# Optimization experiments

Hardware: AMD Instinct MI355X
Metric: run time of the kernel (lower is better)

## Reference

```python
import jax, jax.numpy as jnp
from jax import lax
import numpy as np

V, E, H, L = 32000, 512, 1024, 2
B, S, T = 32, 128, 128
PAD = 0


def _lstm_step(h, c, gates):
    i, f, g, o = jnp.split(gates, 4, axis=-1)
    c_new = jax.nn.sigmoid(f) * c + jax.nn.sigmoid(i) * jnp.tanh(g)
    h_new = jax.nn.sigmoid(o) * jnp.tanh(c_new)
    return h_new, c_new


def _lstm_layer(x_tbe, Wih, Whh, bih, bhh):
    # x_tbe: [T, B, in]; returns hs [T, B, H], final (h, c)
    Bn = x_tbe.shape[1]
    Hn = Whh.shape[1]
    h0 = jnp.zeros((Bn, Hn), x_tbe.dtype)
    c0 = jnp.zeros((Bn, Hn), x_tbe.dtype)

    def step(carry, x_t):
        h, c = carry
        gates = x_t @ Wih.T + h @ Whh.T + (bih + bhh)
        h, c = _lstm_step(h, c, gates)
        return (h, c), h

    (h, c), hs = lax.scan(step, (h0, c0), x_tbe)
    return hs, h, c


def setup_inputs() -> dict:
    key = jax.random.key(0)
    ks = iter(jax.random.split(key, 32))
    s = 0.02

    def p(shape):
        return (jax.random.normal(next(ks), shape, dtype=jnp.float32) * s)

    embed = p((V, E)).at[PAD].set(0.0)  # padding_idx row zeroed
    inp = {
        'src': jax.random.randint(next(ks), (B, S), 0, V),
        'tgt': jax.random.randint(next(ks), (B, T), 0, V),
        'embed': embed,
        'enc_Wih0': p((4 * H, E)), 'enc_Whh0': p((4 * H, H)),
        'enc_bih0': p((4 * H,)), 'enc_bhh0': p((4 * H,)),
        'enc_Wih1': p((4 * H, H)), 'enc_Whh1': p((4 * H, H)),
        'enc_bih1': p((4 * H,)), 'enc_bhh1': p((4 * H,)),
        'dec_Wih': p((4 * H, E + H)), 'dec_Whh': p((4 * H, H)),
        'dec_bih': p((4 * H,)), 'dec_bhh': p((4 * H,)),
        'fc_W': p((V, H)), 'fc_b': p((V,)),
    }
    return inp


def reference(src, tgt, embed, enc_Wih0, enc_Whh0, enc_bih0, enc_bhh0,
              enc_Wih1, enc_Whh1, enc_bih1, enc_bhh1,
              dec_Wih, dec_Whh, dec_bih, dec_bhh, fc_W, fc_b):
    # ----- encoder: 2-layer LSTM -----
    enc_emb = embed[src]                       # [B, S, E]
    x = jnp.transpose(enc_emb, (1, 0, 2))      # [S, B, E]
    hs0, _, _ = _lstm_layer(x, enc_Wih0, enc_Whh0, enc_bih0, enc_bhh0)
    hs1, h_last, c_last = _lstm_layer(hs0, enc_Wih1, enc_Whh1, enc_bih1, enc_bhh1)
    enc_out = jnp.transpose(hs1, (1, 0, 2))    # [B, S, H]

    # ----- decoder: attention + LSTMCell per step -----
    dec_emb = embed[tgt[:, :-1]]               # inputs for steps 1..T-1: [B, T-1, E]
    dec_xs = jnp.transpose(dec_emb, (1, 0, 2)) # [T-1, B, E]

    def dec_step(carry, x_t):
        h, c = carry
        scores = jnp.einsum('bsh,bh->bs', enc_out, h)
        w = jax.nn.softmax(scores, axis=1)
        ctx = jnp.einsum('bs,bsh->bh', w, enc_out)
        xin = jnp.concatenate([x_t, ctx], axis=1)   # [B, E+H]
        gates = xin @ dec_Wih.T + h @ dec_Whh.T + (dec_bih + dec_bhh)
        h, c = _lstm_step(h, c, gates)
        out = h @ fc_W.T + fc_b                     # [B, V]
        return (h, c), out

    _, outs = lax.scan(dec_step, (h_last, c_last), dec_xs)  # [T-1, B, V]
    return jnp.transpose(outs, (1, 0, 2))                   # [B, T-1, V]
```

## Files before the change

### kernel.cpp

```cpp
#include <hip/hip_runtime.h>

typedef unsigned short u16;
typedef __bf16 bf16x8 __attribute__((ext_vector_type(8)));
typedef float f32x4 __attribute__((ext_vector_type(4)));
typedef u16 u16x8 __attribute__((ext_vector_type(8)));
typedef unsigned u32x2 __attribute__((ext_vector_type(2)));

static_assert(sizeof(bf16x8) == 16, "bf16x8 must be 16B");

#define DEV static __device__ __forceinline__

DEV u16 f2bf(float f) {
  unsigned u = __float_as_uint(f);
  u += 0x7FFFu + ((u >> 16) & 1u);
  return (u16)(u >> 16);
}
DEV float bf2f(u16 h) { return __uint_as_float(((unsigned)h) << 16); }
DEV f32x4 mfma16(bf16x8 a, bf16x8 b, f32x4 c) {
  return __builtin_amdgcn_mfma_f32_16x16x32_bf16(a, b, c, 0, 0, 0);
}
DEV bf16x8 ldfrag(const u16* p) { return *reinterpret_cast<const bf16x8*>(p); }
DEV float sigf(float x) { return 1.0f / (1.0f + __expf(-x)); }
DEV bf16x8 asbf(f32x4 v) { union { f32x4 f; bf16x8 h; } u; u.f = v; return u.h; }
DEV void gld16(const void* g, void* l) {
  __builtin_amdgcn_global_load_lds((const __attribute__((address_space(1))) void*)g,
                                   (__attribute__((address_space(3))) void*)l, 16, 0, 0);
}

#define LD16X(i, p) "global_load_dwordx4 %" #i ", %" #p ", off sc0 sc1\n\t"
DEV void ld_a16_coh(const void* p0, const void* p1,
                    f32x4& a0, f32x4& a1, f32x4& a2, f32x4& a3,
                    f32x4& a4, f32x4& a5, f32x4& a6, f32x4& a7,
                    f32x4& b0, f32x4& b1, f32x4& b2, f32x4& b3,
                    f32x4& b4, f32x4& b5, f32x4& b6, f32x4& b7) {
  asm volatile(
      "global_load_dwordx4 %0, %16, off sc0 sc1\n\t"
      "global_load_dwordx4 %1, %16, off offset:64 sc0 sc1\n\t"
      "global_load_dwordx4 %2, %16, off offset:128 sc0 sc1\n\t"
      "global_load_dwordx4 %3, %16, off offset:192 sc0 sc1\n\t"
      "global_load_dwordx4 %4, %16, off offset:256 sc0 sc1\n\t"
      "global_load_dwordx4 %5, %16, off offset:320 sc0 sc1\n\t"
      "global_load_dwordx4 %6, %16, off offset:384 sc0 sc1\n\t"
      "global_load_dwordx4 %7, %16, off offset:448 sc0 sc1\n\t"
      "global_load_dwordx4 %8, %17, off sc0 sc1\n\t"
      "global_load_dwordx4 %9, %17, off offset:64 sc0 sc1\n\t"
      "global_load_dwordx4 %10, %17, off offset:128 sc0 sc1\n\t"
      "global_load_dwordx4 %11, %17, off offset:192 sc0 sc1\n\t"
      "global_load_dwordx4 %12, %17, off offset:256 sc0 sc1\n\t"
      "global_load_dwordx4 %13, %17, off offset:320 sc0 sc1\n\t"
      "global_load_dwordx4 %14, %17, off offset:384 sc0 sc1\n\t"
      "global_load_dwordx4 %15, %17, off offset:448 sc0 sc1\n\t"
      "s_waitcnt vmcnt(0)"
      : "=&v"(a0), "=&v"(a1), "=&v"(a2), "=&v"(a3), "=&v"(a4), "=&v"(a5), "=&v"(a6), "=&v"(a7),
        "=&v"(b0), "=&v"(b1), "=&v"(b2), "=&v"(b3), "=&v"(b4), "=&v"(b5), "=&v"(b6), "=&v"(b7)
      : "v"(p0), "v"(p1)
      : "memory");
}
DEV void ld_a16_coh_nw(const void* p0, const void* p1,
                       f32x4& a0, f32x4& a1, f32x4& a2, f32x4& a3,
                       f32x4& a4, f32x4& a5, f32x4& a6, f32x4& a7,
                       f32x4& b0, f32x4& b1, f32x4& b2, f32x4& b3,
                       f32x4& b4, f32x4& b5, f32x4& b6, f32x4& b7) {
  asm volatile(
      "global_load_dwordx4 %0, %16, off sc0 sc1\n\t"
      "global_load_dwordx4 %1, %16, off offset:64 sc0 sc1\n\t"
      "global_load_dwordx4 %2, %16, off offset:128 sc0 sc1\n\t"
      "global_load_dwordx4 %3, %16, off offset:192 sc0 sc1\n\t"
      "global_load_dwordx4 %4, %16, off offset:256 sc0 sc1\n\t"
      "global_load_dwordx4 %5, %16, off offset:320 sc0 sc1\n\t"
      "global_load_dwordx4 %6, %16, off offset:384 sc0 sc1\n\t"
      "global_load_dwordx4 %7, %16, off offset:448 sc0 sc1\n\t"
      "global_load_dwordx4 %8, %17, off sc0 sc1\n\t"
      "global_load_dwordx4 %9, %17, off offset:64 sc0 sc1\n\t"
      "global_load_dwordx4 %10, %17, off offset:128 sc0 sc1\n\t"
      "global_load_dwordx4 %11, %17, off offset:192 sc0 sc1\n\t"
      "global_load_dwordx4 %12, %17, off offset:256 sc0 sc1\n\t"
      "global_load_dwordx4 %13, %17, off offset:320 sc0 sc1\n\t"
      "global_load_dwordx4 %14, %17, off offset:384 sc0 sc1\n\t"
      "global_load_dwordx4 %15, %17, off offset:448 sc0 sc1"
      : "=&v"(a0), "=&v"(a1), "=&v"(a2), "=&v"(a3), "=&v"(a4), "=&v"(a5), "=&v"(a6), "=&v"(a7),
        "=&v"(b0), "=&v"(b1), "=&v"(b2), "=&v"(b3), "=&v"(b4), "=&v"(b5), "=&v"(b6), "=&v"(b7)
      : "v"(p0), "v"(p1)
      : "memory");
}
DEV f32x4 ld16_coh(const void* p) {
  f32x4 r;
  asm volatile("global_load_dwordx4 %0, %1, off sc0 sc1\n\ts_waitcnt vmcnt(0)"
               : "=&v"(r) : "v"(p) : "memory");
  return r;
}
DEV void ld32_coh(const void* p, f32x4& a, f32x4& b) {
  asm volatile(
      "global_load_dwordx4 %0, %2, off sc0 sc1\n\t"
      "global_load_dwordx4 %1, %2, off offset:16 sc0 sc1\n\t"
      "s_waitcnt vmcnt(0)"
      : "=&v"(a), "=&v"(b) : "v"(p) : "memory");
}
DEV void st32_coh(void* p, unsigned v) {
  asm volatile("global_store_dword %0, %1, off sc0 sc1" ::"v"(p), "v"(v) : "memory");
}
DEV void st8_coh(void* p, unsigned lo, unsigned hi) {
  u32x2 v; v[0] = lo; v[1] = hi;
  asm volatile("global_store_dwordx2 %0, %1, off sc0 sc1" ::"v"(p), "v"(v) : "memory");
}

DEV unsigned ldflag(const unsigned* p) {
  unsigned r;
  asm volatile("global_load_dword %0, %1, off sc0 sc1\n\ts_waitcnt vmcnt(0)"
               : "=&v"(r) : "v"(p) : "memory");
  return r;
}
DEV void poll128(const unsigned* fl, unsigned tgt) {
  if (tgt == 0) return;
  if (threadIdx.x < 64) {
    const unsigned* p0 = fl + (size_t)threadIdx.x * 16;
    const unsigned* p1 = fl + (size_t)(threadIdx.x + 64) * 16;
    for (;;) {
      unsigned a, b;
      asm volatile(
          "global_load_dword %0, %2, off sc0 sc1\n\t"
          "global_load_dword %1, %3, off sc0 sc1\n\t"
          "s_waitcnt vmcnt(0)"
          : "=&v"(a), "=&v"(b) : "v"(p0), "v"(p1) : "memory");
      if (__all((a >= tgt) && (b >= tgt))) break;
      __builtin_amdgcn_s_sleep(1);
    }
  }
  __syncthreads();
}
DEV void poll32(const unsigned* fl, unsigned tgt) {
  if (threadIdx.x < 64) {
    const unsigned* p0 = fl + (size_t)(threadIdx.x & 31) * 16;
    for (;;) {
      unsigned a = ldflag(p0);
      if (__all(a >= tgt)) break;
      __builtin_amdgcn_s_sleep(1);
    }
  }
  __syncthreads();
}
DEV void pollAB(const unsigned* f0, unsigned t0, const unsigned* f1, unsigned t1) {
  const bool n0 = t0 > 0, n1 = t1 > 0;
  if ((n0 || n1) && threadIdx.x < 64) {
    const unsigned* q0 = f0 + (size_t)threadIdx.x * 16;
    const unsigned* q1 = f0 + (size_t)(threadIdx.x + 64) * 16;
    const unsigned* q2 = f1 + (size_t)threadIdx.x * 16;
    const unsigned* q3 = f1 + (size_t)(threadIdx.x + 64) * 16;
    for (;;) {
      unsigned a, b, c, d;
      asm volatile(
          "global_load_dword %0, %4, off sc0 sc1\n\t"
          "global_load_dword %1, %5, off sc0 sc1\n\t"
          "global_load_dword %2, %6, off sc0 sc1\n\t"
          "global_load_dword %3, %7, off sc0 sc1\n\t"
          "s_waitcnt vmcnt(0)"
          : "=&v"(a), "=&v"(b), "=&v"(c), "=&v"(d)
          : "v"(q0), "v"(q1), "v"(q2), "v"(q3) : "memory");
      bool ok = true;
      if (n0) ok = ok && (a >= t0) && (b >= t0);
      if (n1) ok = ok && (c >= t1) && (d >= t1);
      if (__all(ok)) break;
      __builtin_amdgcn_s_sleep(1);
    }
  }
  __syncthreads();
}
DEV void setflag(unsigned* f, unsigned v) {
  asm volatile("s_waitcnt vmcnt(0)" ::: "memory");
  __syncthreads();
  if (threadIdx.x == 0) st32_coh(f, v);
}

#define Bn 32
#define Sn 128
#define Td 127
#define En 512
#define Hn 1024
#define G4 4096
#define Vn 32000

typedef u16 u16x8b __attribute__((ext_vector_type(8)));
__global__ __launch_bounds__(256) void cvt_bf16_kernel(const float* __restrict__ in,
                                                       u16* __restrict__ out, int n8) {
  int gid = blockIdx.x * 256 + threadIdx.x;
  if (gid >= n8) return;
  const float4* ip = (const float4*)in + gid * 2;
  float4 x = ip[0], y = ip[1];
  u16x8b o;
  o[0] = f2bf(x.x); o[1] = f2bf(x.y); o[2] = f2bf(x.z); o[3] = f2bf(x.w);
  o[4] = f2bf(y.x); o[5] = f2bf(y.y); o[6] = f2bf(y.z); o[7] = f2bf(y.w);
  ((u16x8b*)out)[gid] = o;
}

__global__ __launch_bounds__(256) void gather_embed_kernel(const int* __restrict__ idx, int ldidx,
                                                           const float* __restrict__ embed,
                                                           u16* __restrict__ outA, int nrows) {
  int gid = blockIdx.x * 256 + threadIdx.x;
  int total = nrows * (En / 8);
  if (gid >= total) return;
  int r = gid / (En / 8);
  int ck = gid % (En / 8);
  int tcol = r / Bn, b = r % Bn;
  int tok = idx[b * ldidx + tcol];
  const float4* src = (const float4*)(embed + (size_t)tok * En + ck * 8);
  float4 x = src[0], y = src[1];
  u16x8b o;
  o[0] = f2bf(x.x); o[1] = f2bf(x.y); o[2] = f2bf(x.z); o[3] = f2bf(x.w);
  o[4] = f2bf(y.x); o[5] = f2bf(y.y); o[6] = f2bf(y.z); o[7] = f2bf(y.w);
  *(u16x8b*)(outA + (size_t)r * En + ck * 8) = o;
}

__global__ __launch_bounds__(256) void gemm_tile_kernel(const u16* __restrict__ A, int lda,
                                                        const u16* __restrict__ W, int ldw,
                                                        const float* __restrict__ bias0,
                                                        const float* __restrict__ bias1,
                                                        float* __restrict__ Cout, int ldc,
                                                        int Mtiles, int K, int mode) {
  __shared__ u16 Asb[128 * 32];
  __shared__ u16 Bsb[128 * 32];
  int nwg = gridDim.x;
  int cpx = nwg >> 3;
  int bid = ((int)blockIdx.x & 7) * cpx + ((int)blockIdx.x >> 3);
  int mt = bid % Mtiles, nt = bid / Mtiles;
  int tid = threadIdx.x;
  int wave = tid >> 6, lane = tid & 63;
  int lrow = lane & 15, kgrp = lane >> 4;
  int wr = wave >> 1, wc = wave & 1;
  int e0 = wave * 1024 + lane * 8;
  int r0 = e0 >> 5, c0 = e0 & 31;
  int r1 = r0 + 16;
  const u16* Ab = A + (size_t)(mt * 128) * lda;
  const u16* Wb = W + (size_t)(nt * 128) * ldw;
  u16* AsW = Asb + wave * 1024;
  u16* BsW = Bsb + wave * 1024;
  f32x4 acc[4][4] = {};
  for (int k0 = 0; k0 < K; k0 += 32) {
    gld16(Ab + (size_t)r0 * lda + k0 + c0, AsW);
    gld16(Ab + (size_t)r1 * lda + k0 + c0, AsW + 512);
    gld16(Wb + (size_t)r0 * ldw + k0 + c0, BsW);
    gld16(Wb + (size_t)r1 * ldw + k0 + c0, BsW + 512);
    __syncthreads();
    bf16x8 af[4], bfr[4];
#pragma unroll
    for (int i = 0; i < 4; ++i) af[i] = ldfrag(Asb + (wr * 64 + i * 16 + lrow) * 32 + kgrp * 8);
#pragma unroll
    for (int i = 0; i < 4; ++i) bfr[i] = ldfrag(Bsb + (wc * 64 + i * 16 + lrow) * 32 + kgrp * 8);
#pragma unroll
    for (int i = 0; i < 4; ++i)
#pragma unroll
      for (int j = 0; j < 4; ++j) acc[i][j] = mfma16(af[i], bfr[j], acc[i][j]);
    __syncthreads();
  }
  if (mode == 0) {
#pragma unroll
    for (int i = 0; i < 4; ++i) {
      int m = mt * 128 + wr * 64 + i * 16 + kgrp * 4;
#pragma unroll
      for (int j = 0; j < 4; ++j) {
        int n = nt * 128 + wc * 64 + j * 16 + lrow;
        float bb = (bias0 ? bias0[n] : 0.f) + (bias1 ? bias1[n] : 0.f);
#pragma unroll
        for (int r = 0; r < 4; ++r) Cout[(size_t)(m + r) * ldc + n] = acc[i][j][r] + bb;
      }
    }
  } else {
#pragma unroll
    for (int i = 0; i < 4; ++i) {
      int m = mt * 128 + wr * 64 + i * 16 + kgrp * 4;
#pragma unroll
      for (int j = 0; j < 4; ++j) {
        int n = nt * 128 + wc * 64 + j * 16 + lrow;
        float bb = bias0[n];
#pragma unroll
        for (int r = 0; r < 4; ++r) {
          int mm = m + r;
          if (mm < Td * Bn) {
            int tt = mm >> 5, b = mm & 31;
            Cout[((size_t)b * Td + tt) * Vn + n] = acc[i][j][r] + bb;
          }
        }
      }
    }
  }
}

DEV void mm8b(const u16* __restrict__ A0, const char* __restrict__ Wl, int pitchB,
              int kByteBase, int lane, f32x4 acc[2][2]) {
  const int lrow = lane & 15, kgrp = lane >> 4;
  const char* wr0 = Wl + (size_t)lrow * pitchB;
  const char* wr1 = wr0 + (size_t)16 * pitchB;
  const int sw = (lrow & 7) << 4;
  f32x4 s0, s1, s2, s3, s4, s5, s6, s7, u0, u1, u2, u3, u4, u5, u6, u7;
  ld_a16_coh(A0 + (size_t)lrow * 1024 + kgrp * 8, A0 + (size_t)(16 + lrow) * 1024 + kgrp * 8,
             s0, s1, s2, s3, s4, s5, s6, s7, u0, u1, u2, u3, u4, u5, u6, u7);
#define KS(T, U, J, KB)                                                \
  {                                                                    \
    bf16x8 a = asbf(T);                                                \
    int kb = (KB) + (J) * 64 + kgrp * 16;                              \
    bf16x8 w0 = *(const bf16x8*)(wr0 + (size_t)(kb ^ sw));             \
    bf16x8 w1 = *(const bf16x8*)(wr1 + (size_t)(kb ^ sw));             \
    acc[0][0] = mfma16(a, w0, acc[0][0]);                              \
    acc[0][1] = mfma16(a, w1, acc[0][1]);                              \
    bf16x8 cc = asbf(U);                                               \
    acc[1][0] = mfma16(cc, w0, acc[1][0]);                             \
    acc[1][1] = mfma16(cc, w1, acc[1][1]);                             \
  }
  KS(s0, u0, 0, kByteBase) KS(s1, u1, 1, kByteBase) KS(s2, u2, 2, kByteBase)
  KS(s3, u3, 3, kByteBase) KS(s4, u4, 4, kByteBase) KS(s5, u5, 5, kByteBase)
  KS(s6, u6, 6, kByteBase) KS(s7, u7, 7, kByteBase)
}

DEV void mm8b_pair(const u16* __restrict__ A0, const char* __restrict__ Wl, int pitchB,
                   int kByteBase, int lane, f32x4 acc[2][2]) {
  const int lrow = lane & 15, kgrp = lane >> 4;
  const char* wr0 = Wl + (size_t)lrow * pitchB;
  const char* wr1 = wr0 + (size_t)16 * pitchB;
  const int sw = (lrow & 7) << 4;
  f32x4 s0, s1, s2, s3, s4, s5, s6, s7, u0, u1, u2, u3, u4, u5, u6, u7;
  f32x4 t0, t1, t2, t3, t4, t5, t6, t7, v0, v1, v2, v3, v4, v5, v6, v7;
  ld_a16_coh_nw(A0 + (size_t)lrow * 1024 + kgrp * 8, A0 + (size_t)(16 + lrow) * 1024 + kgrp * 8,
                s0, s1, s2, s3, s4, s5, s6, s7, u0, u1, u2, u3, u4, u5, u6, u7);
  ld_a16_coh(A0 + (size_t)lrow * 1024 + 256 + kgrp * 8,
             A0 + (size_t)(16 + lrow) * 1024 + 256 + kgrp * 8,
             t0, t1, t2, t3, t4, t5, t6, t7, v0, v1, v2, v3, v4, v5, v6, v7);
  __builtin_amdgcn_sched_barrier(0);
  KS(s0, u0, 0, kByteBase) KS(s1, u1, 1, kByteBase) KS(s2, u2, 2, kByteBase)
  KS(s3, u3, 3, kByteBase) KS(s4, u4, 4, kByteBase) KS(s5, u5, 5, kByteBase)
  KS(s6, u6, 6, kByteBase) KS(s7, u7, 7, kByteBase)
  KS(t0, v0, 0, kByteBase + 512) KS(t1, v1, 1, kByteBase + 512) KS(t2, v2, 2, kByteBase + 512)
  KS(t3, v3, 3, kByteBase + 512) KS(t4, v4, 4, kByteBase + 512) KS(t5, v5, 5, kByteBase + 512)
  KS(t6, v6, 6, kByteBase + 512) KS(t7, v7, 7, kByteBase + 512)
}

DEV void dump_acc(float* red, f32x4 acc[2][2], int wave, int lane) {
  int lrow = lane & 15, kgrp = lane >> 4;
#pragma unroll
  for (int m = 0; m < 2; ++m)
#pragma unroll
    for (int n = 0; n < 2; ++n)
#pragma unroll
      for (int r = 0; r < 4; ++r)
        red[((((wave * 2 + m) * 2 + n) * 16) + kgrp * 4 + r) * 16 + lrow] = acc[m][n][r];
}
DEV float rsum(const float* red, int m, int n, int rw, int l) {
  float s = 0.f;
#pragma unroll
  for (int w = 0; w < 4; ++w) s += red[((((w * 2 + m) * 2 + n) * 16) + rw) * 16 + l];
  return s;
}
DEV float lstm_apply(const float gs[4], float* c_reg) {
  float ig = sigf(gs[0]), fg = sigf(gs[1]), gg = tanhf(gs[2]), og = sigf(gs[3]);
  float cn = fg * (*c_reg) + ig * gg;
  *c_reg = cn;
  return og * tanhf(cn);
}

__global__ __launch_bounds__(256, 1) void enc_persist8(
    const float* __restrict__ premix, const u16* __restrict__ Whh0, const u16* __restrict__ Wih1,
    const u16* __restrict__ Whh1, const float* __restrict__ bih1, const float* __restrict__ bhh1,
    u16* __restrict__ h0ring, u16* __restrict__ h1ring, float* __restrict__ c1_out,
    u16* __restrict__ enc_b, unsigned* __restrict__ f0, unsigned* __restrict__ f1) {
  extern __shared__ char lds[];
  float* red = (float*)(lds + 131072);
  const int tid = threadIdx.x, wave = tid >> 6, lane = tid & 63;
  const int blk = blockIdx.x;
  const bool l1 = blk >= 128;
  const int base = (blk & 127) * 8;
  if (!l1) {
    for (int i = tid; i < 4096; i += 256) {
      int c = i >> 7;
      int kb = (i & 127) << 4;
      int row = (c >> 3) * Hn + base + (c & 7);
      f32x4 v = *(const f32x4*)(Whh0 + (size_t)row * Hn + (kb >> 1));
      *(f32x4*)(lds + c * 2048 + (kb ^ ((c & 7) << 4))) = v;
    }
  } else {
    for (int i = tid; i < 8192; i += 256) {
      int c = i >> 8;
      int kb = (i & 255) << 4;
      int row = (c >> 3) * Hn + base + (c & 7);
      const u16* src = (kb < 2048) ? (Wih1 + (size_t)row * Hn + (kb >> 1))
                                   : (Whh1 + (size_t)row * Hn + ((kb - 2048) >> 1));
      f32x4 v = *(const f32x4*)src;
      *(f32x4*)(lds + c * 4096 + (kb ^ ((c & 7) << 4))) = v;
    }
  }
  const int b_ = tid >> 3, hc = tid & 7;
  const int m = b_ >> 4, rw = b_ & 15;
  const size_t off = (size_t)b_ * Hn + base + hc;
  float c_reg = 0.f;
  __syncthreads();
  if (!l1) {
    for (int i = 0; i < Sn; ++i) {
      pollAB(f0, (unsigned)i, f1, (i >= 3) ? (unsigned)(i - 2) : 0u);
      const u16* hin = h0ring + (size_t)(i & 3) * (Bn * Hn);
      const float* pmr = premix + (size_t)i * (Bn * G4) + (size_t)b_ * G4 + base + hc;
      float pmv[4];
#pragma unroll
      for (int g = 0; g < 4; ++g) pmv[g] = pmr[(size_t)g * Hn];
      f32x4 acc[2][2] = {};
      mm8b(hin + wave * 256, lds, 2048, wave * 512, lane, acc);
      dump_acc(red, acc, wave, lane);
      __syncthreads();
      float gs[4];
#pragma unroll
      for (int g = 0; g < 4; ++g) {
        int c = g * 8 + hc;
        gs[g] = rsum(red, m, c >> 4, rw, c & 15) + pmv[g];
      }
      float hn = lstm_apply(gs, &c_reg);
      u16 mine = f2bf(hn);
      unsigned nb = (unsigned)(u16)__shfl_xor((int)mine, 1);
      if (!(tid & 1))
        st32_coh(h0ring + (size_t)((i + 1) & 3) * (Bn * Hn) + off,
                 ((unsigned)mine) | (nb << 16));
      setflag(f0 + blk * 16, (unsigned)(i + 1));
    }
  } else {
    float badd[4];
#pragma unroll
    for (int g = 0; g < 4; ++g) badd[g] = bih1[g * Hn + base + hc] + bhh1[g * Hn + base + hc];
    for (int j = 0; j < Sn; ++j) {
      pollAB(f0, (unsigned)(j + 1), f1, (unsigned)j);
      const u16* h0r = h0ring + (size_t)((j + 1) & 3) * (Bn * Hn);
      const u16* h1r = h1ring + (size_t)(j & 1) * (Bn * Hn);
      const u16* srcp = (wave < 2) ? h0r : h1r;
      int ko = (wave & 1) * 512;
      f32x4 acc[2][2] = {};
      mm8b_pair(srcp + ko, lds, 4096, wave * 1024, lane, acc);
      dump_acc(red, acc, wave, lane);
      __syncthreads();
      float gs[4];
#pragma unroll
      for (int g = 0; g < 4; ++g) {
        int c = g * 8 + hc;
        gs[g] = rsum(red, m, c >> 4, rw, c & 15) + badd[g];
      }
      float hn = lstm_apply(gs, &c_reg);
      u16 mine = f2bf(hn);
      unsigned nb = (unsigned)(u16)__shfl_xor((int)mine, 1);
      unsigned packed = ((unsigned)mine) | (nb << 16);
      if (!(tid & 1)) {
        st32_coh(h1ring + (size_t)((j + 1) & 1) * (Bn * Hn) + off, packed);
        *(unsigned*)(enc_b + (size_t)j * (Bn * Hn) + off) = packed;
      }
      if (j == Sn - 1) c1_out[off] = c_reg;
      setflag(f1 + (blk - 128) * 16, (unsigned)(j + 1));
    }
  }
}

__global__ __launch_bounds__(256, 1) void dec_persist10(
    const float* __restrict__ premix, const u16* __restrict__ Wctx, const u16* __restrict__ Whh,
    const float* __restrict__ c_init, u16* __restrict__ hbuf ,
    const u16* __restrict__ enc_b, u16* __restrict__ ctxb, u16* __restrict__ hs_dec,
    unsigned* __restrict__ fg, unsigned* __restrict__ fa) {
  extern __shared__ char lds[];
  const int tid = threadIdx.x, wave = tid >> 6, lane = tid & 63;
  const int blk = blockIdx.x;
  if (blk < 128) {
    float* red = (float*)(lds + 131072);
    const int cg = blk, base = cg * 8;
    for (int i = tid; i < 8192; i += 256) {
      int c = i >> 8;
      int kb = (i & 255) << 4;
      int row = (c >> 3) * Hn + base + (c & 7);
      const u16* src = (kb < 2048) ? (Whh + (size_t)row * Hn + (kb >> 1))
                                   : (Wctx + (size_t)row * 1536 + ((kb - 2048) >> 1));
      f32x4 v = *(const f32x4*)src;
      *(f32x4*)(lds + c * 4096 + (kb ^ ((c & 7) << 4))) = v;
    }
    const int b_ = tid >> 3, hc = tid & 7;
    const int m = b_ >> 4, rw = b_ & 15;
    const size_t off = (size_t)b_ * Hn + base + hc;
    float c_reg = c_init[off];
    __syncthreads();
    for (int t = 0; t < Td; ++t) {
      poll128(fg, (unsigned)t);
      const float* pmr = premix + (size_t)t * (Bn * G4) + (size_t)b_ * G4 + base + hc;
      float pmv[4];
#pragma unroll
      for (int g = 0; g < 4; ++g) pmv[g] = pmr[(size_t)g * Hn];
      f32x4 acc[2][2] = {};
      mm8b(hbuf + (size_t)(t & 1) * (Bn * Hn) + wave * 256, lds, 4096, wave * 512, lane, acc);
      poll32(fa, (unsigned)(t + 1));
      mm8b(ctxb + wave * 256, lds, 4096, 2048 + wave * 512, lane, acc);
      dump_acc(red, acc, wave, lane);
      __syncthreads();
      float gs[4];
#pragma unroll
      for (int g = 0; g < 4; ++g) {
        int c = g * 8 + hc;
        gs[g] = rsum(red, m, c >> 4, rw, c & 15) + pmv[g];
      }
      float hn = lstm_apply(gs, &c_reg);
      u16 mine = f2bf(hn);
      unsigned nb = (unsigned)(u16)__shfl_xor((int)mine, 1);
      unsigned packed = ((unsigned)mine) | (nb << 16);
      if (!(tid & 1)) {
        st32_coh(hbuf + (size_t)((t + 1) & 1) * (Bn * Hn) + off, packed);
        *(unsigned*)(hs_dec + (size_t)t * (Bn * Hn) + off) = packed;
      }
      setflag(fg + cg * 16, (unsigned)(t + 1));
    }
  } else {
    float* scpart = (float*)lds;
    float* scl = (float*)(lds + 33280);
    float* wsm = (float*)(lds + 33792);
    float(*cpart)[16][64] = (float(*)[16][64])(lds + 34304);
    const int b = blk - 128;
    for (int t = 0; t < Td; ++t) {
      poll128(fg, (unsigned)t);
      const u16* hb = hbuf + (size_t)(t & 1) * (Bn * Hn) + (size_t)b * Hn;
      float hf[16];
      {
        union { f32x4 f[2]; u16 u[16]; } U;
        ld32_coh(hb + lane * 16, U.f[0], U.f[1]);
#pragma unroll
        for (int k2 = 0; k2 < 16; ++k2) hf[k2] = bf2f(U.u[k2]);
      }
#pragma unroll 4
      for (int i = 0; i < 32; ++i) {
        int s = wave * 32 + i;
        const u16* er = enc_b + ((size_t)s * Bn + b) * Hn + lane * 16;
        u16x8 e0 = *(const u16x8*)er;
        u16x8 e1 = *(const u16x8*)(er + 8);
        float p2 = 0.f;
#pragma unroll
        for (int k2 = 0; k2 < 8; ++k2) p2 += bf2f(e0[k2]) * hf[k2] + bf2f(e1[k2]) * hf[8 + k2];
        scpart[s * 65 + lane] = p2;
      }
      __syncthreads();
      {
        int s2 = tid >> 1, half = tid & 1;
        const float* pp = scpart + s2 * 65 + half * 32;
        float p = 0.f;
#pragma unroll
        for (int j = 0; j < 32; ++j) p += pp[j];
        p += __shfl_xor(p, 1);
        if (half == 0) scl[s2] = p;
      }
      __syncthreads();
      if (wave == 0) {
        float sa = scl[lane], sb = scl[64 + lane];
        float mx = fmaxf(sa, sb);
#pragma unroll
        for (int o2 = 32; o2; o2 >>= 1) mx = fmaxf(mx, __shfl_xor(mx, o2));
        float ea = __expf(sa - mx), eb = __expf(sb - mx);
        float ss = ea + eb;
#pragma unroll
        for (int o2 = 32; o2; o2 >>= 1) ss += __shfl_xor(ss, o2);
        float inv = 1.0f / ss;
        wsm[lane] = ea * inv;
        wsm[64 + lane] = eb * inv;
      }
      __syncthreads();
      float a0[16];
#pragma unroll
      for (int q = 0; q < 16; ++q) a0[q] = 0.f;
      for (int i = 0; i < 32; ++i) {
        int s = wave * 32 + i;
        float w = wsm[s];
        const u16* er = enc_b + ((size_t)s * Bn + b) * Hn + lane * 16;
        u16x8 e0 = *(const u16x8*)er;
        u16x8 e1 = *(const u16x8*)(er + 8);
#pragma unroll
        for (int q = 0; q < 8; ++q) {
          a0[q] += w * bf2f(e0[q]);
          a0[8 + q] += w * bf2f(e1[q]);
        }
      }
#pragma unroll
      for (int q = 0; q < 16; ++q) cpart[wave][q][lane] = a0[q];
      __syncthreads();
      {
        unsigned pk[2];
#pragma unroll
        for (int h2 = 0; h2 < 2; ++h2) {
          float v0 = 0.f, v1 = 0.f;
          int j0 = tid * 4 + h2 * 2;
#pragma unroll
          for (int w2 = 0; w2 < 4; ++w2) {
            v0 += cpart[w2][j0 & 15][j0 >> 4];
            v1 += cpart[w2][(j0 + 1) & 15][(j0 + 1) >> 4];
          }
          pk[h2] = (unsigned)f2bf(v0) | ((unsigned)f2bf(v1) << 16);
        }
        st8_coh(ctxb + (size_t)b * Hn + tid * 4, pk[0], pk[1]);
      }
      setflag(fa + b * 16, (unsigned)(t + 1));
    }
  }
}

extern "C" void kernel_launch(void* const* d_in, const int* in_sizes, int n_in,
                              void* d_out, int out_size, void* d_ws, size_t ws_size,
                              hipStream_t stream) {
  const int* src = (const int*)d_in[0];
  const int* tgt = (const int*)d_in[1];
  const float* embed = (const float*)d_in[2];
  const float* Wih0 = (const float*)d_in[3];
  const float* Whh0 = (const float*)d_in[4];
  const float* bih0 = (const float*)d_in[5];
  const float* bhh0 = (const float*)d_in[6];
  const float* Wih1 = (const float*)d_in[7];
  const float* Whh1 = (const float*)d_in[8];
  const float* bih1 = (const float*)d_in[9];
  const float* bhh1 = (const float*)d_in[10];
  const float* dWih = (const float*)d_in[11];
  const float* dWhh = (const float*)d_in[12];
  const float* dbih = (const float*)d_in[13];
  const float* dbhh = (const float*)d_in[14];
  const float* fcW = (const float*)d_in[15];
  const float* fcb = (const float*)d_in[16];
  float* out = (float*)d_out;

  (void)hipFuncSetAttribute((const void*)enc_persist8,
                            hipFuncAttributeMaxDynamicSharedMemorySize, 147456);
  (void)hipFuncSetAttribute((const void*)dec_persist10,
                            hipFuncAttributeMaxDynamicSharedMemorySize, 147456);

  char* p = (char*)d_ws;
  auto alloc = [&](size_t bytes) {
    void* r = p;
    p += (bytes + 255) & ~(size_t)255;
    return r;
  };
  u16* Wih0_b = (u16*)alloc((size_t)G4 * En * 2);
  u16* Whh0_b = (u16*)alloc((size_t)G4 * Hn * 2);
  u16* Wih1_b = (u16*)alloc((size_t)G4 * Hn * 2);
  u16* Whh1_b = (u16*)alloc((size_t)G4 * Hn * 2);
  u16* dWih_b = (u16*)alloc((size_t)G4 * 1536 * 2);
  u16* dWhh_b = (u16*)alloc((size_t)G4 * Hn * 2);
  u16* fcW_b = (u16*)alloc((size_t)Vn * Hn * 2);
  u16* embA = (u16*)alloc((size_t)4096 * En * 2);
  float* premix = (float*)alloc((size_t)4096 * G4 * 4);
  u16* enc_b = (u16*)alloc((size_t)Sn * Bn * Hn * 2);
  u16* hs_dec = (u16*)alloc((size_t)4096 * Hn * 2);
  u16* h0ring = (u16*)alloc((size_t)4 * Bn * Hn * 2);
  u16* h1ring = (u16*)alloc((size_t)2 * Bn * Hn * 2);
  float* c1g = (float*)alloc((size_t)Bn * Hn * 4);
  u16* ctx_b = (u16*)alloc((size_t)Bn * Hn * 2);
  unsigned* counters = (unsigned*)alloc(65536);
  unsigned* flagsE0 = counters;
  unsigned* flagsE1 = counters + 2048;
  unsigned* flagsDg = counters + 4096;
  unsigned* flagsDa = counters + 6144;

  auto cvt = [&](const float* in, u16* o, size_t n) {
    int n8 = (int)(n / 8);
    cvt_bf16_kernel<<<(n8 + 255) / 256, 256, 0, stream>>>(in, o, n8);
  };
  cvt(Wih0, Wih0_b, (size_t)G4 * En);
  cvt(Whh0, Whh0_b, (size_t)G4 * Hn);
  cvt(Wih1, Wih1_b, (size_t)G4 * Hn);
  cvt(Whh1, Whh1_b, (size_t)G4 * Hn);
  cvt(dWih, dWih_b, (size_t)G4 * 1536);
  cvt(dWhh, dWhh_b, (size_t)G4 * Hn);
  cvt(fcW, fcW_b, (size_t)Vn * Hn);

  {
    int total = 4096 * (En / 8);
    gather_embed_kernel<<<(total + 255) / 256, 256, 0, stream>>>(src, Sn, embed, embA, Sn * Bn);
    gemm_tile_kernel<<<32 * 32, 256, 0, stream>>>(embA, En, Wih0_b, En, bih0, bhh0, premix, G4,
                                                  32, En, 0);
  }
  (void)hipMemsetAsync(h0ring, 0, (size_t)4 * Bn * Hn * 2, stream);
  (void)hipMemsetAsync(h1ring, 0, (size_t)2 * Bn * Hn * 2, stream);
  (void)hipMemsetAsync(counters, 0, 65536, stream);
  (void)hipMemsetAsync(hs_dec + (size_t)(Td * Bn) * Hn, 0, (size_t)(4096 - Td * Bn) * Hn * 2,
                       stream);

  enc_persist8<<<256, 256, 147456, stream>>>(premix, Whh0_b, Wih1_b, Whh1_b, bih1, bhh1, h0ring,
                                             h1ring, c1g, enc_b, flagsE0, flagsE1);

  {
    int nrows = Td * Bn;
    int total = nrows * (En / 8);
    gather_embed_kernel<<<(total + 255) / 256, 256, 0, stream>>>(tgt, Sn, embed, embA, nrows);
    gemm_tile_kernel<<<32 * 32, 256, 0, stream>>>(embA, En, dWih_b, 1536, dbih, dbhh, premix, G4,
                                                  32, En, 0);
  }

  dec_persist10<<<160, 256, 147456, stream>>>(premix, dWih_b + 512, dWhh_b, c1g,
                                              h1ring , enc_b, ctx_b, hs_dec,
                                              flagsDg, flagsDa);

  gemm_tile_kernel<<<32 * 250, 256, 0, stream>>>(hs_dec, Hn, fcW_b, Hn, fcb, nullptr, out, 0,
                                                 32, Hn, 1);
}
```

Before: 3.251 ms.

## Stage encoder outputs in LDS for decoder attention blocks

```diff
diff --git a/kernel.cpp b/kernel.cpp
--- a/kernel.cpp
+++ b/kernel.cpp
@@ -27,7 +27,6 @@
                                    (__attribute__((address_space(3))) void*)l, 16, 0, 0);
 }
 
-#define LD16X(i, p) "global_load_dwordx4 %" #i ", %" #p ", off sc0 sc1\n\t"
 DEV void ld_a16_coh(const void* p0, const void* p1,
                     f32x4& a0, f32x4& a1, f32x4& a2, f32x4& a3,
                     f32x4& a4, f32x4& a5, f32x4& a6, f32x4& a7,
@@ -89,12 +88,12 @@
                : "=&v"(r) : "v"(p) : "memory");
   return r;
 }
-DEV void ld32_coh(const void* p, f32x4& a, f32x4& b) {
+DEV void ld2x16_coh(const void* p0, const void* p1, f32x4& a, f32x4& b) {
   asm volatile(
       "global_load_dwordx4 %0, %2, off sc0 sc1\n\t"
-      "global_load_dwordx4 %1, %2, off offset:16 sc0 sc1\n\t"
+      "global_load_dwordx4 %1, %3, off sc0 sc1\n\t"
       "s_waitcnt vmcnt(0)"
-      : "=&v"(a), "=&v"(b) : "v"(p) : "memory");
+      : "=&v"(a), "=&v"(b) : "v"(p0), "v"(p1) : "memory");
 }
 DEV void st32_coh(void* p, unsigned v) {
   asm volatile("global_store_dword %0, %1, off sc0 sc1" ::"v"(p), "v"(v) : "memory");
@@ -178,6 +177,7 @@
 #define Hn 1024
 #define G4 4096
 #define Vn 32000
+#define NSTG 63
 
 typedef u16 u16x8b __attribute__((ext_vector_type(8)));
 __global__ __launch_bounds__(256) void cvt_bf16_kernel(const float* __restrict__ in,
@@ -450,7 +450,7 @@
   }
 }
 
-__global__ __launch_bounds__(256, 1) void dec_persist10(
+__global__ __launch_bounds__(256, 1) void dec_persist11(
     const float* __restrict__ premix, const u16* __restrict__ Wctx, const u16* __restrict__ Whh,
     const float* __restrict__ c_init, u16* __restrict__ hbuf ,
     const u16* __restrict__ enc_b, u16* __restrict__ ctxb, u16* __restrict__ hs_dec,
@@ -504,39 +504,46 @@
       setflag(fg + cg * 16, (unsigned)(t + 1));
     }
   } else {
-    float* scpart = (float*)lds;
-    float* scl = (float*)(lds + 33280);
-    float* wsm = (float*)(lds + 33792);
-    float(*cpart)[16][64] = (float(*)[16][64])(lds + 34304);
+    u16* encS = (u16*)lds;
+    float* scl = (float*)(lds + NSTG * 2048);
+    float* wsm = (float*)(lds + NSTG * 2048 + 512);
+    float* scpart = (float*)(lds + NSTG * 2048 + 1024);
+    float(*cpart)[16][64] = (float(*)[16][64])(lds + NSTG * 2048 + 1024);
     const int b = blk - 128;
+    for (int c = tid; c < NSTG * 128; c += 256) {
+      int s = c >> 7, k = c & 127;
+      f32x4 v = *(const f32x4*)(enc_b + ((size_t)s * Bn + b) * Hn + k * 8);
+      *(f32x4*)(encS + (size_t)s * 1024 + k * 8) = v;
+    }
+    __syncthreads();
     for (int t = 0; t < Td; ++t) {
       poll128(fg, (unsigned)t);
       const u16* hb = hbuf + (size_t)(t & 1) * (Bn * Hn) + (size_t)b * Hn;
       float hf[16];
       {
         union { f32x4 f[2]; u16 u[16]; } U;
-        ld32_coh(hb + lane * 16, U.f[0], U.f[1]);
+        ld2x16_coh(hb + lane * 8, hb + 512 + lane * 8, U.f[0], U.f[1]);
 #pragma unroll
         for (int k2 = 0; k2 < 16; ++k2) hf[k2] = bf2f(U.u[k2]);
       }
-#pragma unroll 4
       for (int i = 0; i < 32; ++i) {
         int s = wave * 32 + i;
-        const u16* er = enc_b + ((size_t)s * Bn + b) * Hn + lane * 16;
-        u16x8 e0 = *(const u16x8*)er;
-        u16x8 e1 = *(const u16x8*)(er + 8);
+        const u16* er = (s < NSTG) ? (encS + (size_t)s * 1024)
+                                   : (enc_b + ((size_t)s * Bn + b) * Hn);
+        u16x8 e0 = *(const u16x8*)(er + lane * 8);
+        u16x8 e1 = *(const u16x8*)(er + 512 + lane * 8);
         float p2 = 0.f;
 #pragma unroll
         for (int k2 = 0; k2 < 8; ++k2) p2 += bf2f(e0[k2]) * hf[k2] + bf2f(e1[k2]) * hf[8 + k2];
-        scpart[s * 65 + lane] = p2;
+        p2 += __shfl_xor(p2, 1);
+        p2 += __shfl_xor(p2, 2);
+        if ((lane & 3) == 0) scpart[s * 17 + (lane >> 2)] = p2;
       }
       __syncthreads();
       {
         int s2 = tid >> 1, half = tid & 1;
-        const float* pp = scpart + s2 * 65 + half * 32;
-        float p = 0.f;
-#pragma unroll
-        for (int j = 0; j < 32; ++j) p += pp[j];
+        const float* pp = scpart + s2 * 17 + half * 8;
+        float p = pp[0] + pp[1] + pp[2] + pp[3] + pp[4] + pp[5] + pp[6] + pp[7];
         p += __shfl_xor(p, 1);
         if (half == 0) scl[s2] = p;
       }
@@ -561,9 +568,10 @@
       for (int i = 0; i < 32; ++i) {
         int s = wave * 32 + i;
         float w = wsm[s];
-        const u16* er = enc_b + ((size_t)s * Bn + b) * Hn + lane * 16;
-        u16x8 e0 = *(const u16x8*)er;
-        u16x8 e1 = *(const u16x8*)(er + 8);
+        const u16* er = (s < NSTG) ? (encS + (size_t)s * 1024)
+                                   : (enc_b + ((size_t)s * Bn + b) * Hn);
+        u16x8 e0 = *(const u16x8*)(er + lane * 8);
+        u16x8 e1 = *(const u16x8*)(er + 512 + lane * 8);
 #pragma unroll
         for (int q = 0; q < 8; ++q) {
           a0[q] += w * bf2f(e0[q]);
@@ -577,14 +585,16 @@
         unsigned pk[2];
 #pragma unroll
         for (int h2 = 0; h2 < 2; ++h2) {
-          float v0 = 0.f, v1 = 0.f;
-          int j0 = tid * 4 + h2 * 2;
-#pragma unroll
-          for (int w2 = 0; w2 < 4; ++w2) {
-            v0 += cpart[w2][j0 & 15][j0 >> 4];
-            v1 += cpart[w2][(j0 + 1) & 15][(j0 + 1) >> 4];
+          float vv[2];
+#pragma unroll
+          for (int e2 = 0; e2 < 2; ++e2) {
+            int j = tid * 4 + h2 * 2 + e2;
+            int jj = (j < 512) ? j : (j - 512);
+            int qq = ((j < 512) ? 0 : 8) + (jj & 7);
+            int ll = jj >> 3;
+            vv[e2] = cpart[0][qq][ll] + cpart[1][qq][ll] + cpart[2][qq][ll] + cpart[3][qq][ll];
           }
-          pk[h2] = (unsigned)f2bf(v0) | ((unsigned)f2bf(v1) << 16);
+          pk[h2] = (unsigned)f2bf(vv[0]) | ((unsigned)f2bf(vv[1]) << 16);
         }
         st8_coh(ctxb + (size_t)b * Hn + tid * 4, pk[0], pk[1]);
       }
@@ -617,7 +627,7 @@
 
   (void)hipFuncSetAttribute((const void*)enc_persist8,
                             hipFuncAttributeMaxDynamicSharedMemorySize, 147456);
-  (void)hipFuncSetAttribute((const void*)dec_persist10,
+  (void)hipFuncSetAttribute((const void*)dec_persist11,
                             hipFuncAttributeMaxDynamicSharedMemorySize, 147456);
 
   char* p = (char*)d_ws;
@@ -682,7 +692,7 @@
                                                   32, En, 0);
   }
 
-  dec_persist10<<<160, 256, 147456, stream>>>(premix, dWih_b + 512, dWhh_b, c1g,
+  dec_persist11<<<160, 256, 147456, stream>>>(premix, dWih_b + 512, dWhh_b, c1g,
                                               h1ring , enc_b, ctx_b, hs_dec,
                                               flagsDg, flagsDa);
 
```

Result: slower. 4.351 ms (+33.8%).
